# Optimization experiments

Hardware: AMD Instinct MI355X
Metric: run time of the kernel (lower is better)

## Reference

```python
import jax, jax.numpy as jnp
import numpy as np

NEG_SLOPE = 0.2
LN_EPS = 1e-6

B, L, D, H = 32, 512, 256, 4
N = B * L
E = 65536
C = D  # per-head out channels (GATConv out_channels=d_model)


def setup_inputs() -> dict:
    key = jax.random.key(0)
    ks = jax.random.split(key, 10)
    s = 1.0 / np.sqrt(D)
    inputs = jax.random.normal(ks[0], (B, L, D), dtype=jnp.float32)
    edge_index = jax.random.randint(ks[1], (2, E), 0, N, dtype=jnp.int64)
    return {
        "inputs": inputs,
        "edge_index": edge_index,
        "ln_gamma": jnp.ones((D,), jnp.float32),
        "ln_beta": jnp.zeros((D,), jnp.float32),
        "W1": jax.random.normal(ks[2], (D, D), jnp.float32) * s,   # linear_before_gnn
        "b1": jnp.zeros((D,), jnp.float32),
        "W_gat": jax.random.normal(ks[3], (H * C, D), jnp.float32) * s,  # GATConv.lin (no bias)
        "att_src": jax.random.normal(ks[4], (H, C), jnp.float32) * s,
        "att_dst": jax.random.normal(ks[5], (H, C), jnp.float32) * s,
        "bias_gat": jnp.zeros((C,), jnp.float32),  # concat=False -> size out_channels
        "W2": jax.random.normal(ks[6], (D, D), jnp.float32) * s,   # linear_after_gnn
        "b2": jnp.zeros((D,), jnp.float32),
    }


def _gat_conv(x, edge_index, W_gat, att_src, att_dst, bias_gat):
    # x: [N, D] -> project to [N, H, C]
    xh = (x @ W_gat.T).reshape(N, H, C)
    # add self loops (PyG default add_self_loops=True)
    loops = jnp.arange(N, dtype=edge_index.dtype)
    src = jnp.concatenate([edge_index[0], loops])  # message source j
    dst = jnp.concatenate([edge_index[1], loops])  # message target i
    # per-node attention logits [N, H]
    a_src = jnp.einsum("nhc,hc->nh", xh, att_src)
    a_dst = jnp.einsum("nhc,hc->nh", xh, att_dst)
    # per-edge logits and segment softmax over destination node
    e = jax.nn.leaky_relu(a_src[src] + a_dst[dst], NEG_SLOPE)  # [Etot, H]
    e_max = jax.ops.segment_max(e, dst, num_segments=N)        # every node has a self loop
    e = jnp.exp(e - e_max[dst])
    denom = jax.ops.segment_sum(e, dst, num_segments=N)
    alpha = e / denom[dst]                                     # [Etot, H]
    # weighted message aggregation (dropout on alpha skipped: eval mode)
    msg = xh[src] * alpha[:, :, None]                          # [Etot, H, C]
    out = jax.ops.segment_sum(msg, dst, num_segments=N)        # [N, H, C]
    return out.mean(axis=1) + bias_gat                         # concat=False -> head mean


def reference(inputs, edge_index, ln_gamma, ln_beta, W1, b1, W_gat, att_src, att_dst, bias_gat, W2, b2):
    # LayerNorm(eps=1e-6)
    mu = inputs.mean(-1, keepdims=True)
    var = jnp.mean((inputs - mu) ** 2, axis=-1, keepdims=True)
    x = (inputs - mu) * jax.lax.rsqrt(var + LN_EPS) * ln_gamma + ln_beta
    x = x.reshape(-1, D)
    gnn_in = x @ W1.T + b1
    gnn_out = _gat_conv(gnn_in, edge_index, W_gat, att_src, att_dst, bias_gat)
    y = gnn_out @ W2.T + b2
    # dropout is identity in eval mode; residual add
    return y.reshape(B, L, D) + inputs
```

## Files before the change

### kernel.cpp

```cpp
#include <hip/hip_runtime.h>
#include <math.h>

#define N_NODES 16384
#define D_MODEL 256
#define H_HEADS 4
#define C_CH 256
#define E_EDGES 65536
#define ETOT (E_EDGES + N_NODES)
#define HC 1024

typedef __bf16 bf16x8 __attribute__((ext_vector_type(8)));
typedef __bf16 bf16x4 __attribute__((ext_vector_type(4)));
typedef float f32x4 __attribute__((ext_vector_type(4)));

__device__ __forceinline__ __bf16 f2bf(float f) { return (__bf16)f; }
__device__ __forceinline__ float bf2f(__bf16 b) { return (float)b; }

__global__ __launch_bounds__(256) void prep1_ln(
    const float* __restrict__ Wg, const float* __restrict__ att_src,
    const float* __restrict__ att_dst, const float* __restrict__ W2,
    const int* __restrict__ ei, const float* __restrict__ in,
    const float* __restrict__ gamma, const float* __restrict__ beta,
    float* __restrict__ t, float* __restrict__ V, int* __restrict__ deg,
    __bf16* __restrict__ x_ln)
{
    int b = blockIdx.x;
    int tid = threadIdx.x;
    if (b >= 640) {
        int wave = tid >> 6, lane = tid & 63;
        int row = (b - 640) * 4 + wave;
        float4 v = ((const float4*)(in + (size_t)row * D_MODEL))[lane];
        float s  = v.x + v.y + v.z + v.w;
        float sq = v.x*v.x + v.y*v.y + v.z*v.z + v.w*v.w;
        for (int off = 32; off; off >>= 1) {
            s  += __shfl_xor(s,  off);
            sq += __shfl_xor(sq, off);
        }
        float mean = s * (1.0f / D_MODEL);
        float var  = sq * (1.0f / D_MODEL) - mean * mean;
        float inv  = rsqrtf(var + 1e-6f);
        float4 g = ((const float4*)gamma)[lane];
        float4 bb = ((const float4*)beta)[lane];
        bf16x4 o;
        o[0] = f2bf((v.x - mean) * inv * g.x + bb.x);
        o[1] = f2bf((v.y - mean) * inv * g.y + bb.y);
        o[2] = f2bf((v.z - mean) * inv * g.z + bb.z);
        o[3] = f2bf((v.w - mean) * inv * g.w + bb.w);
        *(bf16x4*)(x_ln + (size_t)row * D_MODEL + lane * 4) = o;
        return;
    }
    if (b < 64) {
        int v = b >> 3, sl = b & 7, h = v & 3;
        const float* att = ((v < 4) ? att_src : att_dst) + h * C_CH;
        float acc = 0.f;
        #pragma unroll
        for (int j = 0; j < 32; ++j) {
            int c = sl * 32 + j;
            acc = fmaf(Wg[(size_t)(h * 256 + c) * 256 + tid], att[c], acc);
        }
        atomicAdd(&t[v * 256 + tid], acc);
    } else if (b < 320) {
        int bb = b - 64;
        int og = (bb & 63) * 4, h = bb >> 6;
        const float* w2r = W2 + (size_t)og * 256;
        const float* wgp = Wg + ((size_t)h * 256) * 256 + tid;
        float a0 = 0.f, a1 = 0.f, a2 = 0.f, a3 = 0.f;
        #pragma unroll 4
        for (int c = 0; c < 256; ++c) {
            float wv = wgp[(size_t)c * 256];
            a0 = fmaf(w2r[c],       wv, a0);
            a1 = fmaf(w2r[256 + c], wv, a1);
            a2 = fmaf(w2r[512 + c], wv, a2);
            a3 = fmaf(w2r[768 + c], wv, a3);
        }
        size_t base = (size_t)og * 1024 + h * 256 + tid;
        V[base]        = a0;
        V[base + 1024] = a1;
        V[base + 2048] = a2;
        V[base + 3072] = a3;
    } else {
        int e = (b - 320) * 256 + tid;
        int dst = (e < E_EDGES) ? ei[E_EDGES + e] : (e - E_EDGES);
        atomicAdd(deg + dst, 1);
    }
}

__global__ __launch_bounds__(256) void prep2(
    const float* __restrict__ t, const float* __restrict__ W1,
    const float* __restrict__ b1, const float* __restrict__ V,
    const float* __restrict__ W2, const float* __restrict__ bg,
    const float* __restrict__ b2, float* __restrict__ u2,
    float* __restrict__ c0, __bf16* __restrict__ Wz,
    float* __restrict__ bias_z, const int* __restrict__ deg,
    int* __restrict__ row_st)
{
    int b = blockIdx.x;
    int d = threadIdx.x;
    if (b < 64) {
        int v = b >> 3, sl = b & 7;
        const float* tv = t + v * 256;
        float acc = 0.f;
        #pragma unroll
        for (int j = 0; j < 32; ++j) {
            int k = sl * 32 + j;
            acc = fmaf(tv[k], W1[(size_t)k * 256 + d], acc);
        }
        atomicAdd(&u2[v * 256 + d], acc);
        if (d < 32) {
            float p = tv[sl * 32 + d] * b1[sl * 32 + d];
            for (int s = 16; s; s >>= 1) p += __shfl_xor(p, s);
            if (d == 0) atomicAdd(&c0[v], p);
        }
        return;
    }
    if (b == 320) {
        __shared__ int wsum[4];
        int lane = d & 63, wid = d >> 6;
        int base = d * 64;
        int run = 0;
        for (int j = 0; j < 64; ++j) run += deg[base + j];
        int x = run;
        #pragma unroll
        for (int off = 1; off < 64; off <<= 1) {
            int y = __shfl_up(x, off);
            if (lane >= off) x += y;
        }
        if (lane == 63) wsum[wid] = x;
        __syncthreads();
        int woff = 0;
        #pragma unroll
        for (int wdx = 0; wdx < 4; ++wdx)
            if (wdx < wid) woff += wsum[wdx];
        int excl = woff + x - run;
        int run2 = 0;
        for (int j = 0; j < 64; ++j) {
            row_st[base + j] = excl + run2;
            run2 += deg[base + j];
        }
        if (d == 255) row_st[N_NODES] = excl + run2;
        return;
    }
    int bb = b - 64;
    int og = (bb & 63) * 4, h = bb >> 6;
    int lane = d & 63, wid = d >> 6;
    const float* vr = V + (size_t)og * 1024 + h * 256;
    float a0 = 0.f, a1 = 0.f, a2 = 0.f, a3 = 0.f;
    #pragma unroll 4
    for (int k = 0; k < 256; ++k) {
        float w1v = W1[(size_t)k * 256 + d];
        a0 = fmaf(vr[k],        w1v, a0);
        a1 = fmaf(vr[1024 + k], w1v, a1);
        a2 = fmaf(vr[2048 + k], w1v, a2);
        a3 = fmaf(vr[3072 + k], w1v, a3);
    }
    size_t base = (size_t)og * 1024 + h * 256 + d;
    Wz[base]        = f2bf(a0);
    Wz[base + 1024] = f2bf(a1);
    Wz[base + 2048] = f2bf(a2);
    Wz[base + 3072] = f2bf(a3);

    __shared__ float red[4][4];
    float b1v = b1[d];
    #pragma unroll
    for (int j = 0; j < 4; ++j) {
        float p = vr[(size_t)j * 1024 + d] * b1v;
        for (int s = 32; s; s >>= 1) p += __shfl_xor(p, s);
        if (lane == 0) red[j][wid] = p;
    }
    __syncthreads();
    if (d < 4) {
        float s = red[d][0] + red[d][1] + red[d][2] + red[d][3];
        atomicAdd(&bias_z[og + d], 0.25f * s);
    }
    if (h == 0) {
        __syncthreads();
        float bgv = bg[d];
        #pragma unroll
        for (int j = 0; j < 4; ++j) {
            float q = W2[(size_t)(og + j) * 256 + d] * bgv;
            for (int s = 32; s; s >>= 1) q += __shfl_xor(q, s);
            if (lane == 0) red[j][wid] = q;
        }
        __syncthreads();
        if (d < 4) {
            float s = red[d][0] + red[d][1] + red[d][2] + red[d][3];
            atomicAdd(&bias_z[og + d], s + b2[og + d]);
        }
    }
}

__global__ __launch_bounds__(256) void logits_scatter(
    const __bf16* __restrict__ x_ln, const float* __restrict__ u2,
    const float* __restrict__ c0, float* __restrict__ a_src,
    float* __restrict__ a_dst, const int* __restrict__ ei,
    const int* __restrict__ row_st, int* __restrict__ cnt,
    int* __restrict__ csr_src)
{
    int b = blockIdx.x;
    int tid = threadIdx.x;
    if (b >= 4096) {
        int e = (b - 4096) * 256 + tid;
        int src, dst;
        if (e < E_EDGES) { src = ei[e]; dst = ei[E_EDGES + e]; }
        else             { src = dst = e - E_EDGES; }
        int pos = atomicAdd(cnt + dst, 1);
        csr_src[row_st[dst] + pos] = src;
        return;
    }
    __shared__ float u2s[8][256];
    __shared__ float c0s[8];
    #pragma unroll
    for (int k = 0; k < 8; ++k) u2s[k][tid] = u2[k * 256 + tid];
    if (tid < 8) c0s[tid] = c0[tid];
    __syncthreads();

    int wave = tid >> 6, lane = tid & 63;
    int n = b * 4 + wave;
    int v = lane >> 3, p = lane & 7;
    const __bf16* xp = x_ln + (size_t)n * D_MODEL + p * 32;
    const float*  up = &u2s[v][p * 32];
    float acc = 0.f;
    #pragma unroll
    for (int ti = 0; ti < 4; ++ti) {
        bf16x8 x = *(const bf16x8*)(xp + ti * 8);
        #pragma unroll
        for (int j = 0; j < 8; ++j)
            acc = fmaf(bf2f(x[j]), up[ti * 8 + j], acc);
    }
    acc += __shfl_xor(acc, 1);
    acc += __shfl_xor(acc, 2);
    acc += __shfl_xor(acc, 4);
    if (p == 0) {
        float o = acc + c0s[v];
        if (v < 4) a_src[n * H_HEADS + v] = o;
        else       a_dst[n * H_HEADS + (v - 4)] = o;
    }
}

__global__ __launch_bounds__(256) void gat_fused(
    const __bf16* __restrict__ x_ln, const float* __restrict__ a_src,
    const float* __restrict__ a_dst, const int* __restrict__ row_start,
    const int* __restrict__ csr_src, __bf16* __restrict__ agg)
{
    int wave = threadIdx.x >> 6, lane = threadIdx.x & 63;
    int i = blockIdx.x * 4 + wave;
    int rs = row_start[i], deg = row_start[i + 1] - rs;
    float4 ad = *(const float4*)(a_dst + i * H_HEADS);

    float acc[4][4] = {};
    float sm0 = 0.f, sm1 = 0.f, sm2 = 0.f, sm3 = 0.f;
    for (int e = 0; e < deg; ++e) {
        int s = csr_src[rs + e];
        float4 as = *(const float4*)(a_src + s * H_HEADS);
        float l0 = as.x + ad.x, l1 = as.y + ad.y, l2 = as.z + ad.z, l3 = as.w + ad.w;
        l0 = (l0 > 0.f) ? l0 : 0.2f * l0;
        l1 = (l1 > 0.f) ? l1 : 0.2f * l1;
        l2 = (l2 > 0.f) ? l2 : 0.2f * l2;
        l3 = (l3 > 0.f) ? l3 : 0.2f * l3;
        float w0 = __expf(l0), w1 = __expf(l1);
        float w2 = __expf(l2), w3 = __expf(l3);
        sm0 += w0; sm1 += w1; sm2 += w2; sm3 += w3;
        bf16x4 x = *(const bf16x4*)(x_ln + (size_t)s * D_MODEL + lane * 4);
        #pragma unroll
        for (int j = 0; j < 4; ++j) {
            float xv = bf2f(x[j]);
            acc[0][j] = fmaf(w0, xv, acc[0][j]);
            acc[1][j] = fmaf(w1, xv, acc[1][j]);
            acc[2][j] = fmaf(w2, xv, acc[2][j]);
            acc[3][j] = fmaf(w3, xv, acc[3][j]);
        }
    }
    float sc[4] = {0.25f / sm0, 0.25f / sm1, 0.25f / sm2, 0.25f / sm3};
    #pragma unroll
    for (int h = 0; h < 4; ++h) {
        bf16x4 o;
        #pragma unroll
        for (int j = 0; j < 4; ++j) o[j] = f2bf(acc[h][j] * sc[h]);
        *(bf16x4*)(agg + (size_t)i * HC + h * 256 + lane * 4) = o;
    }
}

#define GLDP 136

__global__ __launch_bounds__(256) void gemm_skinny(
    const __bf16* __restrict__ A, const __bf16* __restrict__ B,
    const float* __restrict__ bias, const float* __restrict__ resid,
    float* __restrict__ outf, int K)
{
    __shared__ __bf16 As[64 * GLDP];
    __shared__ __bf16 Bs[64 * GLDP];
    int tid  = threadIdx.x;
    int lane = tid & 63;
    int w    = tid >> 6;
    int wm   = w >> 1, wn = w & 1;
    int quad = lane >> 4;
    int l16  = lane & 15;
    int m0 = blockIdx.y * 64;
    int n0 = blockIdx.x * 64;

    f32x4 acc[2][2] = {};

    for (int kb = 0; kb < K; kb += 128) {
        bf16x8 areg[4], breg[4];
        #pragma unroll
        for (int t = 0; t < 4; ++t) {
            int c = tid + t * 256;
            int r = c >> 4, p = c & 15;
            areg[t] = *(const bf16x8*)(A + (size_t)(m0 + r) * K + kb + p * 8);
            breg[t] = *(const bf16x8*)(B + (size_t)(n0 + r) * K + kb + p * 8);
        }
        __syncthreads();
        #pragma unroll
        for (int t = 0; t < 4; ++t) {
            int c = tid + t * 256;
            int r = c >> 4, p = c & 15;
            *(bf16x8*)(As + r * GLDP + p * 8) = areg[t];
            *(bf16x8*)(Bs + r * GLDP + p * 8) = breg[t];
        }
        __syncthreads();
        #pragma unroll
        for (int ks = 0; ks < 4; ++ks) {
            bf16x8 af[2], bfr[2];
            #pragma unroll
            for (int mt = 0; mt < 2; ++mt)
                af[mt] = *(const bf16x8*)(As + (wm * 32 + mt * 16 + l16) * GLDP
                                          + ks * 32 + quad * 8);
            #pragma unroll
            for (int nt = 0; nt < 2; ++nt)
                bfr[nt] = *(const bf16x8*)(Bs + (wn * 32 + nt * 16 + l16) * GLDP
                                           + ks * 32 + quad * 8);
            #pragma unroll
            for (int mt = 0; mt < 2; ++mt)
                #pragma unroll
                for (int nt = 0; nt < 2; ++nt)
                    acc[mt][nt] = __builtin_amdgcn_mfma_f32_16x16x32_bf16(
                        af[mt], bfr[nt], acc[mt][nt], 0, 0, 0);
        }
    }

    int rowb = m0 + wm * 32;
    int colb = n0 + wn * 32;
    #pragma unroll
    for (int nt = 0; nt < 2; ++nt) {
        int col = colb + nt * 16 + l16;
        float bv = bias[col];
        #pragma unroll
        for (int mt = 0; mt < 2; ++mt) {
            int row = rowb + mt * 16 + quad * 4;
            #pragma unroll
            for (int r = 0; r < 4; ++r) {
                size_t off = (size_t)(row + r) * C_CH + col;
                outf[off] = acc[mt][nt][r] + bv + resid[off];
            }
        }
    }
}

extern "C" void kernel_launch(void* const* d_in, const int* in_sizes, int n_in,
                              void* d_out, int out_size, void* d_ws, size_t ws_size,
                              hipStream_t stream)
{
    const float* inp      = (const float*)d_in[0];
    const int*   ei       = (const int*)  d_in[1];
    const float* ln_gamma = (const float*)d_in[2];
    const float* ln_beta  = (const float*)d_in[3];
    const float* W1       = (const float*)d_in[4];
    const float* b1       = (const float*)d_in[5];
    const float* W_gat    = (const float*)d_in[6];
    const float* att_src  = (const float*)d_in[7];
    const float* att_dst  = (const float*)d_in[8];
    const float* bias_gat = (const float*)d_in[9];
    const float* W2       = (const float*)d_in[10];
    const float* b2       = (const float*)d_in[11];

    char* ws = (char*)d_ws;
    __bf16* x_ln_bf   = (__bf16*)(ws);
    __bf16* agg_bf    = (__bf16*)(ws + (8ull  << 20));
    float*  V_f       = (float*)(ws + (40ull << 20));
    __bf16* Wz_b      = (__bf16*)(ws + (41ull << 20));
    float*  a_src_b   = (float*)(ws + (42ull << 20));
    float*  a_dst_b   = a_src_b + (size_t)N_NODES * H_HEADS;
    float*  t_vec     = a_dst_b + (size_t)N_NODES * H_HEADS;
    float*  u2        = t_vec + 8 * 256;
    float*  c0        = u2 + 8 * 256;
    float*  bias_z    = c0 + 8;
    int*    deg       = (int*)(bias_z + 256);
    int*    cnt       = deg + N_NODES;
    int*    row_st    = cnt + N_NODES;
    int*    csr_src   = row_st + N_NODES + 4;

    size_t zbytes = (8 * 256 + 8 * 256 + 8 + 256) * sizeof(float)
                  + 2 * N_NODES * sizeof(int);
    hipMemsetAsync(t_vec, 0, zbytes, stream);

    prep1_ln<<<640 + 4096, 256, 0, stream>>>(W_gat, att_src, att_dst, W2, ei,
                                             inp, ln_gamma, ln_beta,
                                             t_vec, V_f, deg, x_ln_bf);
    prep2<<<321, 256, 0, stream>>>(t_vec, W1, b1, V_f, W2, bias_gat, b2,
                                   u2, c0, Wz_b, bias_z, deg, row_st);
    logits_scatter<<<4096 + 320, 256, 0, stream>>>(x_ln_bf, u2, c0,
                                                   a_src_b, a_dst_b,
                                                   ei, row_st, cnt, csr_src);
    gat_fused<<<N_NODES / 4, 256, 0, stream>>>(x_ln_bf, a_src_b, a_dst_b,
                                               row_st, csr_src, agg_bf);
    gemm_skinny<<<dim3(C_CH / 64, N_NODES / 64), 256, 0, stream>>>(
        agg_bf, Wz_b, bias_z, inp, (float*)d_out, HC);
}
```

Baseline: 185.5 us.

## Retile final GEMM to 64x256 blocks with register double-buffered K loads

The final skinny GEMM is retiled so each block computes a full 64-row by 256-column output tile, with each wave owning a 64x64 sub-tile. The A tile is now read from global memory once per row block instead of four times. K is staged in 64-wide chunks, and the next chunk's global loads are issued into registers before the current chunk is computed, so load latency overlaps MFMA work. The launch grid shrinks to 256 blocks, which leaves fewer blocks to hide latency, and each thread now holds more registers.

```diff
diff --git a/kernel.cpp b/kernel.cpp
--- a/kernel.cpp
+++ b/kernel.cpp
@@ -280,73 +280,105 @@
     }
 }
 
-#define GLDP 136
+#define APAD 72
 
 __global__ __launch_bounds__(256) void gemm_skinny(
     const __bf16* __restrict__ A, const __bf16* __restrict__ B,
     const float* __restrict__ bias, const float* __restrict__ resid,
     float* __restrict__ outf, int K)
 {
-    __shared__ __bf16 As[64 * GLDP];
-    __shared__ __bf16 Bs[64 * GLDP];
+    __shared__ __align__(16) __bf16 As[64 * APAD];
+    __shared__ __align__(16) __bf16 Bs[256 * APAD];
     int tid  = threadIdx.x;
     int lane = tid & 63;
     int w    = tid >> 6;
-    int wm   = w >> 1, wn = w & 1;
     int quad = lane >> 4;
     int l16  = lane & 15;
-    int m0 = blockIdx.y * 64;
-    int n0 = blockIdx.x * 64;
-
-    f32x4 acc[2][2] = {};
-
-    for (int kb = 0; kb < K; kb += 128) {
-        bf16x8 areg[4], breg[4];
-        #pragma unroll
-        for (int t = 0; t < 4; ++t) {
-            int c = tid + t * 256;
-            int r = c >> 4, p = c & 15;
-            areg[t] = *(const bf16x8*)(A + (size_t)(m0 + r) * K + kb + p * 8);
-            breg[t] = *(const bf16x8*)(B + (size_t)(n0 + r) * K + kb + p * 8);
-        }
-        __syncthreads();
-        #pragma unroll
-        for (int t = 0; t < 4; ++t) {
-            int c = tid + t * 256;
-            int r = c >> 4, p = c & 15;
-            *(bf16x8*)(As + r * GLDP + p * 8) = areg[t];
-            *(bf16x8*)(Bs + r * GLDP + p * 8) = breg[t];
-        }
-        __syncthreads();
-        #pragma unroll
-        for (int ks = 0; ks < 4; ++ks) {
-            bf16x8 af[2], bfr[2];
-            #pragma unroll
-            for (int mt = 0; mt < 2; ++mt)
-                af[mt] = *(const bf16x8*)(As + (wm * 32 + mt * 16 + l16) * GLDP
+    int m0 = blockIdx.x * 64;
+    int n0 = w * 64;
+
+    int srow = tid >> 3, sp = tid & 7;
+    const __bf16* Ab = A + (size_t)(m0 + srow) * K + sp * 8;
+    const __bf16* Bb = B + (size_t)srow * K + sp * 8;
+    size_t rstride = (size_t)32 * K;
+
+    f32x4 acc[4][4] = {};
+
+    bf16x8 a0_0, a0_1, b0_[8];
+    bf16x8 a1_0, a1_1, b1_[8];
+
+    auto compute = [&]() {
+        #pragma unroll
+        for (int ks = 0; ks < 2; ++ks) {
+            bf16x8 af[4], bfr[4];
+            #pragma unroll
+            for (int mt = 0; mt < 4; ++mt)
+                af[mt] = *(const bf16x8*)(As + (mt * 16 + l16) * APAD
                                           + ks * 32 + quad * 8);
             #pragma unroll
-            for (int nt = 0; nt < 2; ++nt)
-                bfr[nt] = *(const bf16x8*)(Bs + (wn * 32 + nt * 16 + l16) * GLDP
+            for (int nt = 0; nt < 4; ++nt)
+                bfr[nt] = *(const bf16x8*)(Bs + (n0 + nt * 16 + l16) * APAD
                                            + ks * 32 + quad * 8);
             #pragma unroll
-            for (int mt = 0; mt < 2; ++mt)
+            for (int mt = 0; mt < 4; ++mt)
                 #pragma unroll
-                for (int nt = 0; nt < 2; ++nt)
+                for (int nt = 0; nt < 4; ++nt)
                     acc[mt][nt] = __builtin_amdgcn_mfma_f32_16x16x32_bf16(
                         af[mt], bfr[nt], acc[mt][nt], 0, 0, 0);
         }
-    }
-
-    int rowb = m0 + wm * 32;
-    int colb = n0 + wn * 32;
-    #pragma unroll
-    for (int nt = 0; nt < 2; ++nt) {
-        int col = colb + nt * 16 + l16;
+    };
+
+    a0_0 = *(const bf16x8*)(Ab);
+    a0_1 = *(const bf16x8*)(Ab + rstride);
+    #pragma unroll
+    for (int t = 0; t < 8; ++t)
+        b0_[t] = *(const bf16x8*)(Bb + t * rstride);
+
+    for (int kb = 0; kb < K; kb += 128) {
+        {
+            const __bf16* Ap = Ab + kb + 64;
+            const __bf16* Bp = Bb + kb + 64;
+            a1_0 = *(const bf16x8*)(Ap);
+            a1_1 = *(const bf16x8*)(Ap + rstride);
+            #pragma unroll
+            for (int t = 0; t < 8; ++t)
+                b1_[t] = *(const bf16x8*)(Bp + t * rstride);
+        }
+        __syncthreads();
+        *(bf16x8*)(As + srow * APAD + sp * 8)        = a0_0;
+        *(bf16x8*)(As + (srow + 32) * APAD + sp * 8) = a0_1;
+        #pragma unroll
+        for (int t = 0; t < 8; ++t)
+            *(bf16x8*)(Bs + (srow + t * 32) * APAD + sp * 8) = b0_[t];
+        __syncthreads();
+        compute();
+
+        if (kb + 128 < K) {
+            const __bf16* Ap = Ab + kb + 128;
+            const __bf16* Bp = Bb + kb + 128;
+            a0_0 = *(const bf16x8*)(Ap);
+            a0_1 = *(const bf16x8*)(Ap + rstride);
+            #pragma unroll
+            for (int t = 0; t < 8; ++t)
+                b0_[t] = *(const bf16x8*)(Bp + t * rstride);
+        }
+        __syncthreads();
+        *(bf16x8*)(As + srow * APAD + sp * 8)        = a1_0;
+        *(bf16x8*)(As + (srow + 32) * APAD + sp * 8) = a1_1;
+        #pragma unroll
+        for (int t = 0; t < 8; ++t)
+            *(bf16x8*)(Bs + (srow + t * 32) * APAD + sp * 8) = b1_[t];
+        __syncthreads();
+        compute();
+    }
+
+    #pragma unroll
+    for (int nt = 0; nt < 4; ++nt) {
+        int col = n0 + nt * 16 + l16;
         float bv = bias[col];
         #pragma unroll
-        for (int mt = 0; mt < 2; ++mt) {
-            int row = rowb + mt * 16 + quad * 4;
+        for (int mt = 0; mt < 4; ++mt) {
+            int row = m0 + mt * 16 + quad * 4;
             #pragma unroll
             for (int r = 0; r < 4; ++r) {
                 size_t off = (size_t)(row + r) * C_CH + col;
@@ -403,6 +435,6 @@
                                                    ei, row_st, cnt, csr_src);
     gat_fused<<<N_NODES / 4, 256, 0, stream>>>(x_ln_bf, a_src_b, a_dst_b,
                                                row_st, csr_src, agg_bf);
-    gemm_skinny<<<dim3(C_CH / 64, N_NODES / 64), 256, 0, stream>>>(
-        agg_bf, Wz_b, bias_z, inp, (float*)d_out, HC);
-}
+    gemm_skinny<<<N_NODES / 64, 256, 0, stream>>>(agg_bf, Wz_b, bias_z, inp,
+                                                  (float*)d_out, HC);
+}
```

New measurement: 181.8 us. -2.0%, faster.

## Fuse GAT aggregation with output GEMM via shared-memory tile

Applied to the files above, without the earlier changes.

Merges the per-node attention aggregation kernel and the skinny output GEMM into one kernel. Each block aggregates 32 nodes into a bf16 tile in LDS, then runs MFMA against Wz read directly from global memory, applying bias and residual. This drops the 32 MB agg intermediate write/read and one launch, and unrolls the edge loop by two to overlap gathers. In exchange, each block re-reads the full Wz from global/L2, and the block count drops to 512 with large LDS use, lowering occupancy and latency hiding.

```diff
diff --git a/kernel.cpp b/kernel.cpp
--- a/kernel.cpp
+++ b/kernel.cpp
@@ -237,120 +237,134 @@
     }
 }
 
-__global__ __launch_bounds__(256) void gat_fused(
+#define TPAD 1032
+
+__global__ __launch_bounds__(256) void gat_gemm(
     const __bf16* __restrict__ x_ln, const float* __restrict__ a_src,
     const float* __restrict__ a_dst, const int* __restrict__ row_start,
-    const int* __restrict__ csr_src, __bf16* __restrict__ agg)
+    const int* __restrict__ csr_src, const __bf16* __restrict__ Wz,
+    const float* __restrict__ bias_z, const float* __restrict__ resid,
+    float* __restrict__ outf)
 {
-    int wave = threadIdx.x >> 6, lane = threadIdx.x & 63;
-    int i = blockIdx.x * 4 + wave;
-    int rs = row_start[i], deg = row_start[i + 1] - rs;
-    float4 ad = *(const float4*)(a_dst + i * H_HEADS);
-
-    float acc[4][4] = {};
-    float sm0 = 0.f, sm1 = 0.f, sm2 = 0.f, sm3 = 0.f;
-    for (int e = 0; e < deg; ++e) {
-        int s = csr_src[rs + e];
-        float4 as = *(const float4*)(a_src + s * H_HEADS);
-        float l0 = as.x + ad.x, l1 = as.y + ad.y, l2 = as.z + ad.z, l3 = as.w + ad.w;
-        l0 = (l0 > 0.f) ? l0 : 0.2f * l0;
-        l1 = (l1 > 0.f) ? l1 : 0.2f * l1;
-        l2 = (l2 > 0.f) ? l2 : 0.2f * l2;
-        l3 = (l3 > 0.f) ? l3 : 0.2f * l3;
-        float w0 = __expf(l0), w1 = __expf(l1);
-        float w2 = __expf(l2), w3 = __expf(l3);
-        sm0 += w0; sm1 += w1; sm2 += w2; sm3 += w3;
-        bf16x4 x = *(const bf16x4*)(x_ln + (size_t)s * D_MODEL + lane * 4);
-        #pragma unroll
-        for (int j = 0; j < 4; ++j) {
-            float xv = bf2f(x[j]);
-            acc[0][j] = fmaf(w0, xv, acc[0][j]);
-            acc[1][j] = fmaf(w1, xv, acc[1][j]);
-            acc[2][j] = fmaf(w2, xv, acc[2][j]);
-            acc[3][j] = fmaf(w3, xv, acc[3][j]);
-        }
-    }
-    float sc[4] = {0.25f / sm0, 0.25f / sm1, 0.25f / sm2, 0.25f / sm3};
+    __shared__ __align__(16) __bf16 T[32 * TPAD];
+    int tid = threadIdx.x;
+    int lane = tid & 63, w = tid >> 6;
+    int m0 = blockIdx.x * 32;
+
+    for (int nn = 0; nn < 8; ++nn) {
+        int node = w * 8 + nn;
+        int i = m0 + node;
+        int rs = row_start[i], deg = row_start[i + 1] - rs;
+        float4 ad = *(const float4*)(a_dst + i * H_HEADS);
+
+        float acc[4][4] = {};
+        float sm0 = 0.f, sm1 = 0.f, sm2 = 0.f, sm3 = 0.f;
+        int e = 0;
+        for (; e + 2 <= deg; e += 2) {
+            int s0 = csr_src[rs + e];
+            int s1 = csr_src[rs + e + 1];
+            float4 as0 = *(const float4*)(a_src + s0 * H_HEADS);
+            float4 as1 = *(const float4*)(a_src + s1 * H_HEADS);
+            bf16x4 x0 = *(const bf16x4*)(x_ln + (size_t)s0 * D_MODEL + lane * 4);
+            bf16x4 x1 = *(const bf16x4*)(x_ln + (size_t)s1 * D_MODEL + lane * 4);
+            float l00 = as0.x + ad.x, l01 = as0.y + ad.y,
+                  l02 = as0.z + ad.z, l03 = as0.w + ad.w;
+            float l10 = as1.x + ad.x, l11 = as1.y + ad.y,
+                  l12 = as1.z + ad.z, l13 = as1.w + ad.w;
+            l00 = (l00 > 0.f) ? l00 : 0.2f * l00;
+            l01 = (l01 > 0.f) ? l01 : 0.2f * l01;
+            l02 = (l02 > 0.f) ? l02 : 0.2f * l02;
+            l03 = (l03 > 0.f) ? l03 : 0.2f * l03;
+            l10 = (l10 > 0.f) ? l10 : 0.2f * l10;
+            l11 = (l11 > 0.f) ? l11 : 0.2f * l11;
+            l12 = (l12 > 0.f) ? l12 : 0.2f * l12;
+            l13 = (l13 > 0.f) ? l13 : 0.2f * l13;
+            float w00 = __expf(l00), w01 = __expf(l01),
+                  w02 = __expf(l02), w03 = __expf(l03);
+            float w10 = __expf(l10), w11 = __expf(l11),
+                  w12 = __expf(l12), w13 = __expf(l13);
+            sm0 += w00 + w10; sm1 += w01 + w11;
+            sm2 += w02 + w12; sm3 += w03 + w13;
+            #pragma unroll
+            for (int j = 0; j < 4; ++j) {
+                float xv0 = bf2f(x0[j]);
+                float xv1 = bf2f(x1[j]);
+                acc[0][j] = fmaf(w00, xv0, acc[0][j]);
+                acc[1][j] = fmaf(w01, xv0, acc[1][j]);
+                acc[2][j] = fmaf(w02, xv0, acc[2][j]);
+                acc[3][j] = fmaf(w03, xv0, acc[3][j]);
+                acc[0][j] = fmaf(w10, xv1, acc[0][j]);
+                acc[1][j] = fmaf(w11, xv1, acc[1][j]);
+                acc[2][j] = fmaf(w12, xv1, acc[2][j]);
+                acc[3][j] = fmaf(w13, xv1, acc[3][j]);
+            }
+        }
+        if (e < deg) {
+            int s = csr_src[rs + e];
+            float4 as = *(const float4*)(a_src + s * H_HEADS);
+            bf16x4 x = *(const bf16x4*)(x_ln + (size_t)s * D_MODEL + lane * 4);
+            float l0 = as.x + ad.x, l1 = as.y + ad.y,
+                  l2 = as.z + ad.z, l3 = as.w + ad.w;
+            l0 = (l0 > 0.f) ? l0 : 0.2f * l0;
+            l1 = (l1 > 0.f) ? l1 : 0.2f * l1;
+            l2 = (l2 > 0.f) ? l2 : 0.2f * l2;
+            l3 = (l3 > 0.f) ? l3 : 0.2f * l3;
+            float w0 = __expf(l0), w1 = __expf(l1);
+            float w2 = __expf(l2), w3 = __expf(l3);
+            sm0 += w0; sm1 += w1; sm2 += w2; sm3 += w3;
+            #pragma unroll
+            for (int j = 0; j < 4; ++j) {
+                float xv = bf2f(x[j]);
+                acc[0][j] = fmaf(w0, xv, acc[0][j]);
+                acc[1][j] = fmaf(w1, xv, acc[1][j]);
+                acc[2][j] = fmaf(w2, xv, acc[2][j]);
+                acc[3][j] = fmaf(w3, xv, acc[3][j]);
+            }
+        }
+        float sc[4] = {0.25f / sm0, 0.25f / sm1, 0.25f / sm2, 0.25f / sm3};
+        #pragma unroll
+        for (int h = 0; h < 4; ++h) {
+            bf16x4 o;
+            #pragma unroll
+            for (int j = 0; j < 4; ++j) o[j] = f2bf(acc[h][j] * sc[h]);
+            *(bf16x4*)(T + node * TPAD + h * 256 + lane * 4) = o;
+        }
+    }
+    __syncthreads();
+
+    int quad = lane >> 4, l16 = lane & 15;
+    int n0 = w * 64;
+    f32x4 pacc[2][4] = {};
+    #pragma unroll 4
+    for (int kk = 0; kk < HC; kk += 32) {
+        bf16x8 af[2], bfr[4];
+        #pragma unroll
+        for (int mt = 0; mt < 2; ++mt)
+            af[mt] = *(const bf16x8*)(T + (mt * 16 + l16) * TPAD
+                                      + kk + quad * 8);
+        #pragma unroll
+        for (int nt = 0; nt < 4; ++nt)
+            bfr[nt] = *(const bf16x8*)(Wz + (size_t)(n0 + nt * 16 + l16) * HC
+                                       + kk + quad * 8);
+        #pragma unroll
+        for (int mt = 0; mt < 2; ++mt)
+            #pragma unroll
+            for (int nt = 0; nt < 4; ++nt)
+                pacc[mt][nt] = __builtin_amdgcn_mfma_f32_16x16x32_bf16(
+                    af[mt], bfr[nt], pacc[mt][nt], 0, 0, 0);
+    }
+
     #pragma unroll
-    for (int h = 0; h < 4; ++h) {
-        bf16x4 o;
-        #pragma unroll
-        for (int j = 0; j < 4; ++j) o[j] = f2bf(acc[h][j] * sc[h]);
-        *(bf16x4*)(agg + (size_t)i * HC + h * 256 + lane * 4) = o;
-    }
-}
-
-#define GLDP 136
-
-__global__ __launch_bounds__(256) void gemm_skinny(
-    const __bf16* __restrict__ A, const __bf16* __restrict__ B,
-    const float* __restrict__ bias, const float* __restrict__ resid,
-    float* __restrict__ outf, int K)
-{
-    __shared__ __bf16 As[64 * GLDP];
-    __shared__ __bf16 Bs[64 * GLDP];
-    int tid  = threadIdx.x;
-    int lane = tid & 63;
-    int w    = tid >> 6;
-    int wm   = w >> 1, wn = w & 1;
-    int quad = lane >> 4;
-    int l16  = lane & 15;
-    int m0 = blockIdx.y * 64;
-    int n0 = blockIdx.x * 64;
-
-    f32x4 acc[2][2] = {};
-
-    for (int kb = 0; kb < K; kb += 128) {
-        bf16x8 areg[4], breg[4];
-        #pragma unroll
-        for (int t = 0; t < 4; ++t) {
-            int c = tid + t * 256;
-            int r = c >> 4, p = c & 15;
-            areg[t] = *(const bf16x8*)(A + (size_t)(m0 + r) * K + kb + p * 8);
-            breg[t] = *(const bf16x8*)(B + (size_t)(n0 + r) * K + kb + p * 8);
-        }
-        __syncthreads();
-        #pragma unroll
-        for (int t = 0; t < 4; ++t) {
-            int c = tid + t * 256;
-            int r = c >> 4, p = c & 15;
-            *(bf16x8*)(As + r * GLDP + p * 8) = areg[t];
-            *(bf16x8*)(Bs + r * GLDP + p * 8) = breg[t];
-        }
-        __syncthreads();
-        #pragma unroll
-        for (int ks = 0; ks < 4; ++ks) {
-            bf16x8 af[2], bfr[2];
-            #pragma unroll
-            for (int mt = 0; mt < 2; ++mt)
-                af[mt] = *(const bf16x8*)(As + (wm * 32 + mt * 16 + l16) * GLDP
-                                          + ks * 32 + quad * 8);
-            #pragma unroll
-            for (int nt = 0; nt < 2; ++nt)
-                bfr[nt] = *(const bf16x8*)(Bs + (wn * 32 + nt * 16 + l16) * GLDP
-                                           + ks * 32 + quad * 8);
-            #pragma unroll
-            for (int mt = 0; mt < 2; ++mt)
-                #pragma unroll
-                for (int nt = 0; nt < 2; ++nt)
-                    acc[mt][nt] = __builtin_amdgcn_mfma_f32_16x16x32_bf16(
-                        af[mt], bfr[nt], acc[mt][nt], 0, 0, 0);
-        }
-    }
-
-    int rowb = m0 + wm * 32;
-    int colb = n0 + wn * 32;
-    #pragma unroll
-    for (int nt = 0; nt < 2; ++nt) {
-        int col = colb + nt * 16 + l16;
-        float bv = bias[col];
+    for (int nt = 0; nt < 4; ++nt) {
+        int col = n0 + nt * 16 + l16;
+        float bv = bias_z[col];
         #pragma unroll
         for (int mt = 0; mt < 2; ++mt) {
-            int row = rowb + mt * 16 + quad * 4;
+            int row = m0 + mt * 16 + quad * 4;
             #pragma unroll
             for (int r = 0; r < 4; ++r) {
                 size_t off = (size_t)(row + r) * C_CH + col;
-                outf[off] = acc[mt][nt][r] + bv + resid[off];
+                outf[off] = pacc[mt][nt][r] + bv + resid[off];
             }
         }
     }
@@ -375,7 +389,6 @@
 
     char* ws = (char*)d_ws;
     __bf16* x_ln_bf   = (__bf16*)(ws);
-    __bf16* agg_bf    = (__bf16*)(ws + (8ull  << 20));
     float*  V_f       = (float*)(ws + (40ull << 20));
     __bf16* Wz_b      = (__bf16*)(ws + (41ull << 20));
     float*  a_src_b   = (float*)(ws + (42ull << 20));
@@ -401,8 +414,7 @@
     logits_scatter<<<4096 + 320, 256, 0, stream>>>(x_ln_bf, u2, c0,
                                                    a_src_b, a_dst_b,
                                                    ei, row_st, cnt, csr_src);
-    gat_fused<<<N_NODES / 4, 256, 0, stream>>>(x_ln_bf, a_src_b, a_dst_b,
-                                               row_st, csr_src, agg_bf);
-    gemm_skinny<<<dim3(C_CH / 64, N_NODES / 64), 256, 0, stream>>>(
-        agg_bf, Wz_b, bias_z, inp, (float*)d_out, HC);
+    gat_gemm<<<N_NODES / 32, 256, 0, stream>>>(x_ln_bf, a_src_b, a_dst_b,
+                                               row_st, csr_src, Wz_b, bias_z,
+                                               inp, (float*)d_out);
 }
```

New measurement: 197.0 us. +6.2%, slower.
